# Kernel optimization log

Measured on AMD Instinct MI355X. Metric: run time of the kernel, lower is better.

## Reference

```python
import jax, jax.numpy as jnp
import numpy as np
import math

NH = 16  # n_head
HS = 64  # head_size = n_embd // n_head


def setup_inputs() -> dict:
    key = jax.random.key(0)
    ks = jax.random.split(key, 7)
    B, T, C, QL, KVL = 2, 2048, 1024, 128, 128
    s = lambda k, shape, fan_in: jax.random.normal(k, shape, jnp.float32) / np.sqrt(fan_in)
    return {
        "x": jax.random.normal(ks[0], (B, T, C), jnp.float32),
        "W_dq": s(ks[1], (QL, C), C),
        "W_uq": s(ks[2], (C, QL), QL),
        "W_dkv": s(ks[3], (KVL, C), C),
        "W_uk": s(ks[4], (C, KVL), KVL),
        "W_uv": s(ks[5], (C, KVL), KVL),
        "W_o": s(ks[6], (C, C), C),
    }


def reference(x, W_dq, W_uq, W_dkv, W_uk, W_uv, W_o):
    B, T, C = x.shape
    kvl = W_dkv.shape[0]
    # absorbed matrices (training branch)
    k_eff = (W_dq.T @ W_uq.T @ W_uk).reshape(NH, HS, kvl)            # (nh, hs, kvl)
    v_eff = (W_uv.T @ W_o.T).reshape(kvl, NH, HS).transpose(1, 0, 2)  # (nh, kvl, hs)
    # latent kv cache
    c_kv = x @ W_dkv.T                                                # (B, T, kvl)
    # query path
    q = (x @ W_dq.T @ W_uq.T).reshape(B, T, NH, HS).transpose(0, 2, 1, 3)  # (B, nh, T, hs)
    # scores: q @ k_eff @ c_kv^T
    ql = jnp.einsum('bhtd,hdl->bhtl', q, k_eff)                       # (B, nh, T, kvl)
    scores = jnp.einsum('bhtl,bsl->bhts', ql, c_kv) / math.sqrt(HS)   # (B, nh, T, T)
    # causal mask
    mask = jnp.tril(jnp.ones((T, T), dtype=bool))
    scores = jnp.where(mask[None, None], scores, -jnp.inf)
    attn = jax.nn.softmax(scores, axis=-1)
    # output: attn @ c_kv @ v_eff
    ctx = jnp.einsum('bhts,bsl->bhtl', attn, c_kv)                    # (B, nh, T, kvl)
    y = jnp.einsum('bhtl,hld->bhtd', ctx, v_eff)                      # (B, nh, T, hs)
    y = y.transpose(0, 2, 1, 3).reshape(B, T, C)
    return y, c_kv
```

## Files before the change

kernel.cpp:

```cpp
#include <hip/hip_runtime.h>
#include <hip/hip_bf16.h>

typedef __hip_bfloat16 bf16;
typedef __attribute__((ext_vector_type(8))) short short8;
typedef __attribute__((ext_vector_type(4))) float f32x4;

#define NHD 16
#define HSD 64
#define KVLD 128
#define QLD 128
#define CD 1024
#define BD 2
#define TD 2048

__device__ __forceinline__ short8 ld8(const bf16* p) { return *(const short8*)p; }
__device__ __forceinline__ void st8(bf16* p, short8 v) { *(short8*)p = v; }

__device__ __forceinline__ void st4(bf16* p, float4 a) {
    union { short4 s; bf16 h[4]; } u;
    u.h[0] = __float2bfloat16(a.x); u.h[1] = __float2bfloat16(a.y);
    u.h[2] = __float2bfloat16(a.z); u.h[3] = __float2bfloat16(a.w);
    *(short4*)p = u.s;
}
__device__ __forceinline__ void st4f(bf16* p, f32x4 a) {
    union { short4 s; bf16 h[4]; } u;
    u.h[0] = __float2bfloat16(a[0]); u.h[1] = __float2bfloat16(a[1]);
    u.h[2] = __float2bfloat16(a[2]); u.h[3] = __float2bfloat16(a[3]);
    *(short4*)p = u.s;
}

__global__ __launch_bounds__(256) void k_pre(const float* __restrict__ wuq,
                                             const float* __restrict__ wuk,
                                             const float* __restrict__ wdq,
                                             const float* __restrict__ wdkv,
                                             float* __restrict__ m1p,
                                             float* __restrict__ G,
                                             bf16* __restrict__ wqkv_bf) {
    const int b = blockIdx.x;
    const int tid = threadIdx.x;
    if (b < 128) {
        const int part = b >> 4, ig = b & 15;
        const int i = ig * 8 + (tid >> 5);
        const int j4 = (tid & 31) << 2;
        const float* wq = wuq + (size_t)part * 128 * QLD;
        const float* wk = wuk + (size_t)part * 128 * KVLD;
        float4 acc = make_float4(0.f, 0.f, 0.f, 0.f);
        for (int c0 = 0; c0 < 128; c0 += 8) {
            float a[8]; float4 kv[8];
#pragma unroll
            for (int u = 0; u < 8; ++u) {
                a[u] = wq[(c0 + u) * QLD + i];
                kv[u] = *(const float4*)(wk + (c0 + u) * KVLD + j4);
            }
#pragma unroll
            for (int u = 0; u < 8; ++u) {
                acc.x = fmaf(a[u], kv[u].x, acc.x);
                acc.y = fmaf(a[u], kv[u].y, acc.y);
                acc.z = fmaf(a[u], kv[u].z, acc.z);
                acc.w = fmaf(a[u], kv[u].w, acc.w);
            }
        }
        *(float4*)(m1p + (size_t)part * 16384 + (size_t)i * 128 + j4) = acc;
    } else if (b < 256) {
        const int b1 = b - 128;
        const int h = b1 >> 3, p8 = b1 & 7;
        const int p = p8 * 16 + (tid >> 4);
        const int i8 = (tid & 15) << 3;
        float acc[8];
#pragma unroll
        for (int t = 0; t < 8; ++t) acc[t] = 0.f;
        const float* wdqp = wdq + (size_t)p * CD + h * 64;
        const float* wuqh = wuq + (size_t)(h * 64) * QLD + i8;
        for (int d0 = 0; d0 < 64; d0 += 4) {
            float a[4]; float4 b0[4], b1v[4];
#pragma unroll
            for (int u = 0; u < 4; ++u) {
                a[u] = wdqp[d0 + u];
                b0[u] = *(const float4*)(wuqh + (d0 + u) * QLD);
                b1v[u] = *(const float4*)(wuqh + (d0 + u) * QLD + 4);
            }
#pragma unroll
            for (int u = 0; u < 4; ++u) {
                acc[0] = fmaf(a[u], b0[u].x, acc[0]);  acc[1] = fmaf(a[u], b0[u].y, acc[1]);
                acc[2] = fmaf(a[u], b0[u].z, acc[2]);  acc[3] = fmaf(a[u], b0[u].w, acc[3]);
                acc[4] = fmaf(a[u], b1v[u].x, acc[4]); acc[5] = fmaf(a[u], b1v[u].y, acc[5]);
                acc[6] = fmaf(a[u], b1v[u].z, acc[6]); acc[7] = fmaf(a[u], b1v[u].w, acc[7]);
            }
        }
        float* dst = G + (size_t)h * 16384 + (size_t)p * 128 + i8;
        *(float4*)dst = make_float4(acc[0], acc[1], acc[2], acc[3]);
        *(float4*)(dst + 4) = make_float4(acc[4], acc[5], acc[6], acc[7]);
    } else {
        const int r = (b - 256) * 4 + (tid >> 6);
        const int lane = tid & 63;
        const float* src = (r < 128) ? (wdq + (size_t)r * CD) : (wdkv + (size_t)(r - 128) * CD);
        float4 f[4];
#pragma unroll
        for (int k = 0; k < 4; ++k) f[k] = ((const float4*)src)[lane + k * 64];
#pragma unroll
        for (int k = 0; k < 4; ++k)
            st4(wqkv_bf + (size_t)r * CD + (lane + k * 64) * 4, f[k]);
    }
}

__global__ __launch_bounds__(256) void k_main(const float* __restrict__ x,
                                              const bf16* __restrict__ wqkv_bf,
                                              const float* __restrict__ m1p,
                                              const float* __restrict__ G,
                                              const float* __restrict__ wuv,
                                              const float* __restrict__ wo,
                                              bf16* __restrict__ q1_bf,
                                              float* __restrict__ ckv_out,
                                              bf16* __restrict__ ckv_bf,
                                              bf16* __restrict__ ckvT_bf,
                                              bf16* __restrict__ Et_bf,
                                              bf16* __restrict__ veffT_bf) {
    __shared__ __align__(16) char arena[49152];
    const int blk = blockIdx.x;
    const int tid = threadIdx.x;

    if (blk < 256) {
        const int m0 = blk * 16;
        const int w = tid >> 6, lane = tid & 63, m16 = lane & 15, g = lane >> 4;
        bf16* As = (bf16*)arena;
        bf16* Bs = (bf16*)(arena + 2304);

        const int arow = tid >> 4, akc = (tid & 15) << 2;
        const float* axp = x + (size_t)(m0 + arow) * CD + akc;
        int brow[8], bkc[8];
#pragma unroll
        for (int kk = 0; kk < 8; ++kk) {
            int v = tid + kk * 256;
            brow[kk] = v >> 3; bkc[kk] = (v & 7) << 3;
        }

        float4 pA = *(const float4*)(axp);
        short8 pB[8];
#pragma unroll
        for (int kk = 0; kk < 8; ++kk)
            pB[kk] = ld8(wqkv_bf + (size_t)brow[kk] * CD + bkc[kk]);

        f32x4 acc[4];
#pragma unroll
        for (int nb = 0; nb < 4; ++nb) acc[nb] = (f32x4){0.f, 0.f, 0.f, 0.f};

        for (int k0 = 0; k0 < CD; k0 += 64) {
            __syncthreads();
            st4(As + arow * 72 + akc, pA);
#pragma unroll
            for (int kk = 0; kk < 8; ++kk)
                st8(Bs + brow[kk] * 72 + bkc[kk], pB[kk]);
            __syncthreads();
            if (k0 + 64 < CD) {
                pA = *(const float4*)(axp + k0 + 64);
#pragma unroll
                for (int kk = 0; kk < 8; ++kk)
                    pB[kk] = ld8(wqkv_bf + (size_t)brow[kk] * CD + k0 + 64 + bkc[kk]);
            }
            short8 aF[2];
#pragma unroll
            for (int kf = 0; kf < 2; ++kf)
                aF[kf] = ld8(As + m16 * 72 + kf * 32 + g * 8);
#pragma unroll
            for (int nb = 0; nb < 4; ++nb)
#pragma unroll
                for (int kf = 0; kf < 2; ++kf) {
                    short8 bF = ld8(Bs + (w * 64 + nb * 16 + m16) * 72 + kf * 32 + g * 8);
                    acc[nb] = __builtin_amdgcn_mfma_f32_16x16x32_bf16(aF[kf], bF, acc[nb], 0, 0, 0);
                }
        }

#pragma unroll
        for (int nb = 0; nb < 4; ++nb)
#pragma unroll
            for (int r = 0; r < 4; ++r) {
                int t = m0 + g * 4 + r;
                int col = w * 64 + nb * 16 + m16;
                float v = acc[nb][r];
                if (col < 128) {
                    q1_bf[(size_t)t * QLD + col] = __float2bfloat16(v);
                } else {
                    int l = col - 128;
                    ckv_out[(size_t)t * KVLD + l] = v;
                    bf16 hv = __float2bfloat16(v);
                    ckv_bf[(size_t)t * KVLD + l] = hv;
                    int b = t >> 11, tl = t & 2047;
                    ckvT_bf[((size_t)b * KVLD + l) * TD + tl] = hv;
                }
            }
    } else if (blk < 512) {
        const int b2 = blk - 256;
        const int h = b2 >> 4, lb = b2 & 15;
        float* m1s = (float*)arena;
        for (int v = tid; v < 1024; v += 256) {
            int p = v >> 3, lq = v & 7;
            float s = 0.f;
#pragma unroll
            for (int part = 0; part < 8; ++part)
                s += m1p[(size_t)part * 16384 + (size_t)p * 128 + lb * 8 + lq];
            m1s[v] = s;
        }
        __syncthreads();
        const int lq = tid >> 5, i4 = (tid & 31) << 2;
        const float* Gh = G + (size_t)h * 16384;
        float4 acc = make_float4(0.f, 0.f, 0.f, 0.f);
        for (int p0 = 0; p0 < 128; p0 += 8) {
            float4 g[8]; float a[8];
#pragma unroll
            for (int u = 0; u < 8; ++u) {
                g[u] = *(const float4*)(Gh + (p0 + u) * 128 + i4);
                a[u] = m1s[(p0 + u) * 8 + lq];
            }
#pragma unroll
            for (int u = 0; u < 8; ++u) {
                acc.x = fmaf(a[u], g[u].x, acc.x);
                acc.y = fmaf(a[u], g[u].y, acc.y);
                acc.z = fmaf(a[u], g[u].z, acc.z);
                acc.w = fmaf(a[u], g[u].w, acc.w);
            }
        }
        const float sc = 0.1803368801f;
        const int l = lb * 8 + lq;
        st4(Et_bf + ((size_t)h * 128 + l) * 128 + i4,
            make_float4(sc * acc.x, sc * acc.y, sc * acc.z, sc * acc.w));
    } else {
        const int b3 = blk - 512;
        const int cc0 = b3 * 4;
        float* woS = (float*)arena;
        float* wuvS = (float*)arena + 4096;
#pragma unroll
        for (int k = 0; k < 4; ++k)
            ((float4*)woS)[tid + k * 256] = ((const float4*)(wo + (size_t)cc0 * CD))[tid + k * 256];

        const int r = tid >> 6;
        const int lh = tid & 63;
        float4 pf[8];
#pragma unroll
        for (int t = 0; t < 8; ++t)
            pf[t] = ((const float4*)wuv)[t * 256 + tid];

        float a0 = 0.f, a1 = 0.f;
        for (int ch = 0; ch < 16; ++ch) {
            __syncthreads();
#pragma unroll
            for (int t = 0; t < 8; ++t)
                ((float4*)wuvS)[t * 256 + tid] = pf[t];
            __syncthreads();
            if (ch < 15) {
#pragma unroll
                for (int t = 0; t < 8; ++t)
                    pf[t] = ((const float4*)wuv)[(ch + 1) * 2048 + t * 256 + tid];
            }
            const float* wr = woS + r * 1024 + ch * 64;
            const float2* vv = (const float2*)wuvS + lh;
#pragma unroll 16
            for (int cc = 0; cc < 64; ++cc) {
                float wv = wr[cc];
                float2 v = vv[cc * 64];
                a0 = fmaf(wv, v.x, a0);
                a1 = fmaf(wv, v.y, a1);
            }
        }
        union { short2 s; bf16 h2[2]; } u;
        u.h2[0] = __float2bfloat16(a0);
        u.h2[1] = __float2bfloat16(a1);
        *(short2*)(veffT_bf + (size_t)(cc0 + r) * KVLD + lh * 2) = u.s;
    }
}

__global__ __launch_bounds__(512, 4) void k_flash(const bf16* __restrict__ Q1_bf,
                                                  const bf16* __restrict__ Et_bf,
                                                  const bf16* __restrict__ ckv_bf,
                                                  const bf16* __restrict__ ckvT_bf,
                                                  const bf16* __restrict__ veffT_bf,
                                                  float* __restrict__ yout) {
    const int h = blockIdx.x & 15;
    const int b = blockIdx.x >> 4;
    const int qlo = blockIdx.y;
    const int qhi = 31 - qlo;
    const int tid = threadIdx.x;
    const int w = tid >> 6;
    const int ws = w >> 2;
    const int wq = w & 3;
    const int lane = tid & 63;
    const int m16 = lane & 15;
    const int g = lane >> 4;
    const int myqt = ws ? qlo : qhi;
    const int row0 = myqt * 64;

    __shared__ __align__(16) short smem_raw[28288];
    bf16* smem = (bf16*)smem_raw;
    bf16* kvN = smem;
    bf16* kvT = smem + 8704;
    bf16* pS  = smem + 19072 + w * 1152;
    bf16* bufLo = kvT;
    bf16* vT = smem + 19072;

    {
        const bf16 one = __float2bfloat16(1.0f);
        for (int idx = tid; idx < 16 * 72; idx += 512)
            kvT[9216 + idx] = one;
    }

    {
        const bf16* q1hi = Q1_bf + ((size_t)(b * TD + qhi * 64)) * QLD;
        const bf16* q1lo = Q1_bf + ((size_t)(b * TD + qlo * 64)) * QLD;
#pragma unroll
        for (int k = 0; k < 2; ++k) {
            int v = tid + k * 512;
            int row = v >> 4, cv = (v & 15) << 3;
            st8(kvN + row * 136 + cv, ld8(q1hi + row * QLD + cv));
            st8(bufLo + row * 136 + cv, ld8(q1lo + row * QLD + cv));
        }
    }
    __syncthreads();
    bf16* myQ1 = ws ? bufLo : kvN;
    {
        short8 aq[4];
#pragma unroll
        for (int kf = 0; kf < 4; ++kf)
            aq[kf] = ld8(myQ1 + (wq * 16 + m16) * 136 + kf * 32 + g * 8);
        const bf16* Eh = Et_bf + (size_t)h * QLD * KVLD;
        f32x4 qc[8];
#pragma unroll
        for (int nb = 0; nb < 8; ++nb) qc[nb] = (f32x4){0.f, 0.f, 0.f, 0.f};
#pragma unroll
        for (int nb = 0; nb < 8; ++nb)
#pragma unroll
            for (int kf = 0; kf < 4; ++kf) {
                short8 bq = ld8(Eh + (nb * 16 + m16) * QLD + kf * 32 + g * 8);
                qc[nb] = __builtin_amdgcn_mfma_f32_16x16x32_bf16(aq[kf], bq, qc[nb], 0, 0, 0);
            }
        __syncthreads();
#pragma unroll
        for (int nb = 0; nb < 8; ++nb)
#pragma unroll
            for (int r = 0; r < 4; ++r)
                myQ1[(wq * 16 + g * 4 + r) * 136 + nb * 16 + m16] = __float2bfloat16(qc[nb][r]);
    }
    __syncthreads();
    short8 qlA[4];
#pragma unroll
    for (int kf = 0; kf < 4; ++kf)
        qlA[kf] = ld8(myQ1 + (wq * 16 + m16) * 136 + kf * 32 + g * 8);

    f32x4 cx[9];
#pragma unroll
    for (int nb = 0; nb < 9; ++nb) cx[nb] = (f32x4){0.f, 0.f, 0.f, 0.f};
    float mrow = -INFINITY;
    const int rg = row0 + wq * 16 + m16;

    const bf16* ckb = ckv_bf + (size_t)b * TD * KVLD;
    const bf16* ckTb = ckvT_bf + (size_t)b * KVLD * TD;

    int nrow[2], ncol[2], trow[2], tcol[2];
#pragma unroll
    for (int k = 0; k < 2; ++k) {
        int v = tid + k * 512;
        nrow[k] = v >> 4; ncol[k] = (v & 15) << 3;
        trow[k] = v >> 3; tcol[k] = (v & 7) << 3;
    }
    short8 pfN[2], pfT[2];
#pragma unroll
    for (int k = 0; k < 2; ++k) {
        pfN[k] = ld8(ckb + (size_t)nrow[k] * KVLD + ncol[k]);
        pfT[k] = ld8(ckTb + (size_t)trow[k] * TD + tcol[k]);
    }

    for (int tile = 0; tile <= qhi; ++tile) {
        const int s0 = tile * 64;
        __syncthreads();
#pragma unroll
        for (int k = 0; k < 2; ++k) {
            st8(kvN + nrow[k] * 136 + ncol[k], pfN[k]);
            st8(kvT + trow[k] * 72 + tcol[k], pfT[k]);
        }
        __syncthreads();
        if (tile < qhi) {
            const int s1 = s0 + 64;
#pragma unroll
            for (int k = 0; k < 2; ++k) {
                pfN[k] = ld8(ckb + (size_t)(s1 + nrow[k]) * KVLD + ncol[k]);
                pfT[k] = ld8(ckTb + (size_t)trow[k] * TD + s1 + tcol[k]);
            }
        }

        if (ws == 0 || tile <= qlo) {
            f32x4 sa[4];
#pragma unroll
            for (int nb = 0; nb < 4; ++nb) sa[nb] = (f32x4){0.f, 0.f, 0.f, 0.f};
#pragma unroll
            for (int nb = 0; nb < 4; ++nb)
#pragma unroll
                for (int kf = 0; kf < 4; ++kf) {
                    short8 ak = ld8(kvN + (nb * 16 + m16) * 136 + kf * 32 + g * 8);
                    sa[nb] = __builtin_amdgcn_mfma_f32_16x16x32_bf16(ak, qlA[kf], sa[nb], 0, 0, 0);
                }

            if (tile == myqt) {
#pragma unroll
                for (int nb = 0; nb < 4; ++nb)
#pragma unroll
                    for (int r = 0; r < 4; ++r) {
                        int sg = s0 + nb * 16 + g * 4 + r;
                        if (sg > rg) sa[nb][r] = -INFINITY;
                    }
            }

            float mloc = sa[0][0];
#pragma unroll
            for (int nb = 0; nb < 4; ++nb)
#pragma unroll
                for (int r = 0; r < 4; ++r) mloc = fmaxf(mloc, sa[nb][r]);
            mloc = fmaxf(mloc, __shfl_xor(mloc, 16));
            mloc = fmaxf(mloc, __shfl_xor(mloc, 32));
            if (__any(mloc > mrow)) {
                float mt = fmaxf(mrow, mloc);
                float al = exp2f(mrow - mt);
                mrow = mt;
#pragma unroll
                for (int nb = 0; nb < 9; ++nb)
#pragma unroll
                    for (int r = 0; r < 4; ++r) cx[nb][r] *= al;
            }

#pragma unroll
            for (int nb = 0; nb < 4; ++nb) {
                float4 p4;
                p4.x = exp2f(sa[nb][0] - mrow);
                p4.y = exp2f(sa[nb][1] - mrow);
                p4.z = exp2f(sa[nb][2] - mrow);
                p4.w = exp2f(sa[nb][3] - mrow);
                st4(pS + m16 * 72 + nb * 16 + g * 4, p4);
            }
            __builtin_amdgcn_wave_barrier();

            short8 pA[2];
#pragma unroll
            for (int kf = 0; kf < 2; ++kf)
                pA[kf] = ld8(pS + m16 * 72 + kf * 32 + g * 8);
#pragma unroll
            for (int nb = 0; nb < 9; ++nb)
#pragma unroll
                for (int kf = 0; kf < 2; ++kf) {
                    short8 av = ld8(kvT + (nb * 16 + m16) * 72 + kf * 32 + g * 8);
                    cx[nb] = __builtin_amdgcn_mfma_f32_16x16x32_bf16(av, pA[kf], cx[nb], 0, 0, 0);
                }
        }
    }

    float invl = 1.f / cx[8][0];
#pragma unroll
    for (int nb = 0; nb < 8; ++nb)
#pragma unroll
        for (int r = 0; r < 4; ++r) cx[nb][r] *= invl;
    __syncthreads();
    bf16* ctxS = ws ? bufLo : kvN;
#pragma unroll
    for (int nb = 0; nb < 8; ++nb)
        st4f(ctxS + (wq * 16 + m16) * 136 + nb * 16 + g * 4, cx[nb]);
    {
        const bf16* vsrc = veffT_bf + (size_t)h * HSD * KVLD;
#pragma unroll
        for (int k = 0; k < 2; ++k) {
            int v = tid + k * 512;
            int row = v >> 4, cv = (v & 15) << 3;
            st8(vT + row * 136 + cv, ld8(vsrc + row * KVLD + cv));
        }
    }
    __syncthreads();

    short8 cB[4];
#pragma unroll
    for (int kf = 0; kf < 4; ++kf)
        cB[kf] = ld8(ctxS + (wq * 16 + m16) * 136 + kf * 32 + g * 8);
    f32x4 ya[4];
#pragma unroll
    for (int nb = 0; nb < 4; ++nb) ya[nb] = (f32x4){0.f, 0.f, 0.f, 0.f};
#pragma unroll
    for (int nb = 0; nb < 4; ++nb)
#pragma unroll
        for (int kf = 0; kf < 4; ++kf) {
            short8 av = ld8(vT + (nb * 16 + m16) * 136 + kf * 32 + g * 8);
            ya[nb] = __builtin_amdgcn_mfma_f32_16x16x32_bf16(av, cB[kf], ya[nb], 0, 0, 0);
        }
    float* yo = yout + ((size_t)b * TD + rg) * CD + h * HSD;
#pragma unroll
    for (int nb = 0; nb < 4; ++nb)
        *(float4*)(yo + nb * 16 + g * 4) = *(float4*)&ya[nb];
}

extern "C" void kernel_launch(void* const* d_in, const int* in_sizes, int n_in,
                              void* d_out, int out_size, void* d_ws, size_t ws_size,
                              hipStream_t stream) {
    const float* x    = (const float*)d_in[0];
    const float* wdq  = (const float*)d_in[1];
    const float* wuq  = (const float*)d_in[2];
    const float* wdkv = (const float*)d_in[3];
    const float* wuk  = (const float*)d_in[4];
    const float* wuv  = (const float*)d_in[5];
    const float* wo   = (const float*)d_in[6];
    float* yout = (float*)d_out;
    float* ckv_out = yout + (size_t)BD * TD * CD;

    float* ws = (float*)d_ws;
    float* M1P = ws;
    float* G   = M1P + 131072;
    bf16* wqkv_bf  = (bf16*)(G + 262144);
    bf16* Et_bf    = wqkv_bf + 262144;
    bf16* veffT_bf = Et_bf + 262144;
    bf16* ckv_bf   = veffT_bf + 131072;
    bf16* ckvT_bf  = ckv_bf + 524288;
    bf16* Q1_bf    = ckvT_bf + 524288;

    k_pre <<<320, 256, 0, stream>>>(wuq, wuk, wdq, wdkv, M1P, G, wqkv_bf);
    k_main<<<768, 256, 0, stream>>>(x, wqkv_bf, M1P, G, wuv, wo,
                                    Q1_bf, ckv_out, ckv_bf, ckvT_bf, Et_bf, veffT_bf);

    dim3 grid(32, 16);
    k_flash<<<grid, 512, 0, stream>>>(Q1_bf, Et_bf, ckv_bf, ckvT_bf, veffT_bf, yout);
}
```

Baseline: 226.1 us.

## Fuse weight preprocessing kernel into main projection kernel, removing a launch

Removes the separate k_pre launch. The projection blocks now read fp32 W_dq/W_dkv directly and convert to bf16 on the fly. The E-matrix blocks recompute the Wuq^T·Wuk product and the per-head G tile locally in shared memory instead of reading partial sums from global memory. This drops one kernel launch and its global round trips, at the cost of redundant per-block recomputation: each of the 256 E blocks does a 1024-long reduction plus a G tile computation.

```diff
diff --git a/kernel.cpp b/kernel.cpp
--- a/kernel.cpp
+++ b/kernel.cpp
@@ -16,6 +16,14 @@
 __device__ __forceinline__ short8 ld8(const bf16* p) { return *(const short8*)p; }
 __device__ __forceinline__ void st8(bf16* p, short8 v) { *(short8*)p = v; }
 
+__device__ __forceinline__ short8 cvt8(float4 a, float4 b) {
+    union { short8 s; bf16 h[8]; } u;
+    u.h[0] = __float2bfloat16(a.x); u.h[1] = __float2bfloat16(a.y);
+    u.h[2] = __float2bfloat16(a.z); u.h[3] = __float2bfloat16(a.w);
+    u.h[4] = __float2bfloat16(b.x); u.h[5] = __float2bfloat16(b.y);
+    u.h[6] = __float2bfloat16(b.z); u.h[7] = __float2bfloat16(b.w);
+    return u.s;
+}
 __device__ __forceinline__ void st4(bf16* p, float4 a) {
     union { short4 s; bf16 h[4]; } u;
     u.h[0] = __float2bfloat16(a.x); u.h[1] = __float2bfloat16(a.y);
@@ -29,92 +37,19 @@
     *(short4*)p = u.s;
 }
 
-__global__ __launch_bounds__(256) void k_pre(const float* __restrict__ wuq,
+__global__ __launch_bounds__(256) void k_aux(const float* __restrict__ x,
+                                             const float* __restrict__ wdq,
+                                             const float* __restrict__ wuq,
+                                             const float* __restrict__ wdkv,
                                              const float* __restrict__ wuk,
-                                             const float* __restrict__ wdq,
-                                             const float* __restrict__ wdkv,
-                                             float* __restrict__ m1p,
-                                             float* __restrict__ G,
-                                             bf16* __restrict__ wqkv_bf) {
-    const int b = blockIdx.x;
-    const int tid = threadIdx.x;
-    if (b < 128) {
-        const int part = b >> 4, ig = b & 15;
-        const int i = ig * 8 + (tid >> 5);
-        const int j4 = (tid & 31) << 2;
-        const float* wq = wuq + (size_t)part * 128 * QLD;
-        const float* wk = wuk + (size_t)part * 128 * KVLD;
-        float4 acc = make_float4(0.f, 0.f, 0.f, 0.f);
-        for (int c0 = 0; c0 < 128; c0 += 8) {
-            float a[8]; float4 kv[8];
-#pragma unroll
-            for (int u = 0; u < 8; ++u) {
-                a[u] = wq[(c0 + u) * QLD + i];
-                kv[u] = *(const float4*)(wk + (c0 + u) * KVLD + j4);
-            }
-#pragma unroll
-            for (int u = 0; u < 8; ++u) {
-                acc.x = fmaf(a[u], kv[u].x, acc.x);
-                acc.y = fmaf(a[u], kv[u].y, acc.y);
-                acc.z = fmaf(a[u], kv[u].z, acc.z);
-                acc.w = fmaf(a[u], kv[u].w, acc.w);
-            }
-        }
-        *(float4*)(m1p + (size_t)part * 16384 + (size_t)i * 128 + j4) = acc;
-    } else if (b < 256) {
-        const int b1 = b - 128;
-        const int h = b1 >> 3, p8 = b1 & 7;
-        const int p = p8 * 16 + (tid >> 4);
-        const int i8 = (tid & 15) << 3;
-        float acc[8];
-#pragma unroll
-        for (int t = 0; t < 8; ++t) acc[t] = 0.f;
-        const float* wdqp = wdq + (size_t)p * CD + h * 64;
-        const float* wuqh = wuq + (size_t)(h * 64) * QLD + i8;
-        for (int d0 = 0; d0 < 64; d0 += 4) {
-            float a[4]; float4 b0[4], b1v[4];
-#pragma unroll
-            for (int u = 0; u < 4; ++u) {
-                a[u] = wdqp[d0 + u];
-                b0[u] = *(const float4*)(wuqh + (d0 + u) * QLD);
-                b1v[u] = *(const float4*)(wuqh + (d0 + u) * QLD + 4);
-            }
-#pragma unroll
-            for (int u = 0; u < 4; ++u) {
-                acc[0] = fmaf(a[u], b0[u].x, acc[0]);  acc[1] = fmaf(a[u], b0[u].y, acc[1]);
-                acc[2] = fmaf(a[u], b0[u].z, acc[2]);  acc[3] = fmaf(a[u], b0[u].w, acc[3]);
-                acc[4] = fmaf(a[u], b1v[u].x, acc[4]); acc[5] = fmaf(a[u], b1v[u].y, acc[5]);
-                acc[6] = fmaf(a[u], b1v[u].z, acc[6]); acc[7] = fmaf(a[u], b1v[u].w, acc[7]);
-            }
-        }
-        float* dst = G + (size_t)h * 16384 + (size_t)p * 128 + i8;
-        *(float4*)dst = make_float4(acc[0], acc[1], acc[2], acc[3]);
-        *(float4*)(dst + 4) = make_float4(acc[4], acc[5], acc[6], acc[7]);
-    } else {
-        const int r = (b - 256) * 4 + (tid >> 6);
-        const int lane = tid & 63;
-        const float* src = (r < 128) ? (wdq + (size_t)r * CD) : (wdkv + (size_t)(r - 128) * CD);
-        float4 f[4];
-#pragma unroll
-        for (int k = 0; k < 4; ++k) f[k] = ((const float4*)src)[lane + k * 64];
-#pragma unroll
-        for (int k = 0; k < 4; ++k)
-            st4(wqkv_bf + (size_t)r * CD + (lane + k * 64) * 4, f[k]);
-    }
-}
-
-__global__ __launch_bounds__(256) void k_main(const float* __restrict__ x,
-                                              const bf16* __restrict__ wqkv_bf,
-                                              const float* __restrict__ m1p,
-                                              const float* __restrict__ G,
-                                              const float* __restrict__ wuv,
-                                              const float* __restrict__ wo,
-                                              bf16* __restrict__ q1_bf,
-                                              float* __restrict__ ckv_out,
-                                              bf16* __restrict__ ckv_bf,
-                                              bf16* __restrict__ ckvT_bf,
-                                              bf16* __restrict__ Et_bf,
-                                              bf16* __restrict__ veffT_bf) {
+                                             const float* __restrict__ wuv,
+                                             const float* __restrict__ wo,
+                                             bf16* __restrict__ q1_bf,
+                                             float* __restrict__ ckv_out,
+                                             bf16* __restrict__ ckv_bf,
+                                             bf16* __restrict__ ckvT_bf,
+                                             bf16* __restrict__ Et_bf,
+                                             bf16* __restrict__ veffT_bf) {
     __shared__ __align__(16) char arena[49152];
     const int blk = blockIdx.x;
     const int tid = threadIdx.x;
@@ -128,17 +63,22 @@
         const int arow = tid >> 4, akc = (tid & 15) << 2;
         const float* axp = x + (size_t)(m0 + arow) * CD + akc;
         int brow[8], bkc[8];
+        const float* bsrc[8];
 #pragma unroll
         for (int kk = 0; kk < 8; ++kk) {
             int v = tid + kk * 256;
             brow[kk] = v >> 3; bkc[kk] = (v & 7) << 3;
+            bsrc[kk] = ((brow[kk] < 128) ? (wdq + (size_t)brow[kk] * CD)
+                                         : (wdkv + (size_t)(brow[kk] - 128) * CD)) + bkc[kk];
         }
 
         float4 pA = *(const float4*)(axp);
-        short8 pB[8];
-#pragma unroll
-        for (int kk = 0; kk < 8; ++kk)
-            pB[kk] = ld8(wqkv_bf + (size_t)brow[kk] * CD + bkc[kk]);
+        float4 pB0[8], pB1[8];
+#pragma unroll
+        for (int kk = 0; kk < 8; ++kk) {
+            pB0[kk] = *(const float4*)(bsrc[kk]);
+            pB1[kk] = *(const float4*)(bsrc[kk] + 4);
+        }
 
         f32x4 acc[4];
 #pragma unroll
@@ -149,13 +89,15 @@
             st4(As + arow * 72 + akc, pA);
 #pragma unroll
             for (int kk = 0; kk < 8; ++kk)
-                st8(Bs + brow[kk] * 72 + bkc[kk], pB[kk]);
+                st8(Bs + brow[kk] * 72 + bkc[kk], cvt8(pB0[kk], pB1[kk]));
             __syncthreads();
             if (k0 + 64 < CD) {
                 pA = *(const float4*)(axp + k0 + 64);
 #pragma unroll
-                for (int kk = 0; kk < 8; ++kk)
-                    pB[kk] = ld8(wqkv_bf + (size_t)brow[kk] * CD + k0 + 64 + bkc[kk]);
+                for (int kk = 0; kk < 8; ++kk) {
+                    pB0[kk] = *(const float4*)(bsrc[kk] + k0 + 64);
+                    pB1[kk] = *(const float4*)(bsrc[kk] + k0 + 68);
+                }
             }
             short8 aF[2];
 #pragma unroll
@@ -190,39 +132,87 @@
             }
     } else if (blk < 512) {
         const int b2 = blk - 256;
-        const int h = b2 >> 4, lb = b2 & 15;
+        const int h = b2 >> 4;
+        const int lb = b2 & 15;
         float* m1s = (float*)arena;
-        for (int v = tid; v < 1024; v += 256) {
-            int p = v >> 3, lq = v & 7;
-            float s = 0.f;
-#pragma unroll
-            for (int part = 0; part < 8; ++part)
-                s += m1p[(size_t)part * 16384 + (size_t)p * 128 + lb * 8 + lq];
-            m1s[v] = s;
-        }
-        __syncthreads();
-        const int lq = tid >> 5, i4 = (tid & 31) << 2;
-        const float* Gh = G + (size_t)h * 16384;
-        float4 acc = make_float4(0.f, 0.f, 0.f, 0.f);
-        for (int p0 = 0; p0 < 128; p0 += 8) {
-            float4 g[8]; float a[8];
-#pragma unroll
-            for (int u = 0; u < 8; ++u) {
-                g[u] = *(const float4*)(Gh + (p0 + u) * 128 + i4);
-                a[u] = m1s[(p0 + u) * 8 + lq];
-            }
-#pragma unroll
-            for (int u = 0; u < 8; ++u) {
-                acc.x = fmaf(a[u], g[u].x, acc.x);
-                acc.y = fmaf(a[u], g[u].y, acc.y);
-                acc.z = fmaf(a[u], g[u].z, acc.z);
-                acc.w = fmaf(a[u], g[u].w, acc.w);
-            }
+        float* gS  = (float*)(arena + 4096);
+
+        {
+            const int p = tid >> 1;
+            const int lh = tid & 1;
+            const int l0 = lb * 8 + lh * 4;
+            const float* wq = wuq + p;
+            const float* wk = wuk + l0;
+            float4 A = make_float4(0.f, 0.f, 0.f, 0.f);
+            for (int c0 = 0; c0 < CD; c0 += 4) {
+                float a[4]; float4 v[4];
+#pragma unroll
+                for (int u = 0; u < 4; ++u) {
+                    a[u] = wq[(c0 + u) * QLD];
+                    v[u] = *(const float4*)(wk + (c0 + u) * KVLD);
+                }
+#pragma unroll
+                for (int u = 0; u < 4; ++u) {
+                    A.x = fmaf(a[u], v[u].x, A.x); A.y = fmaf(a[u], v[u].y, A.y);
+                    A.z = fmaf(a[u], v[u].z, A.z); A.w = fmaf(a[u], v[u].w, A.w);
+                }
+            }
+            *(float4*)(m1s + p * 8 + lh * 4) = A;
+        }
+
+        const int le = tid >> 5;
+        const int i4 = (tid & 31) << 2;
+        float4 E = make_float4(0.f, 0.f, 0.f, 0.f);
+
+#pragma unroll 1
+        for (int ph = 0; ph < 2; ++ph) {
+            {
+                const int pl = tid >> 2;
+                const int i0 = (tid & 3) << 5;
+                const float* wa = wdq + (size_t)(ph * 64 + pl) * CD + h * 64;
+                const float* wb = wuq + (size_t)(h * 64) * QLD + i0;
+                float4 Gc[8];
+#pragma unroll
+                for (int t = 0; t < 8; ++t) Gc[t] = make_float4(0.f, 0.f, 0.f, 0.f);
+                for (int d = 0; d < 64; ++d) {
+                    float a = wa[d];
+                    float4 r[8];
+#pragma unroll
+                    for (int t = 0; t < 8; ++t)
+                        r[t] = *(const float4*)(wb + d * QLD + t * 4);
+#pragma unroll
+                    for (int t = 0; t < 8; ++t) {
+                        Gc[t].x = fmaf(a, r[t].x, Gc[t].x);
+                        Gc[t].y = fmaf(a, r[t].y, Gc[t].y);
+                        Gc[t].z = fmaf(a, r[t].z, Gc[t].z);
+                        Gc[t].w = fmaf(a, r[t].w, Gc[t].w);
+                    }
+                }
+                float* gd = gS + pl * 128 + i0;
+#pragma unroll
+                for (int t = 0; t < 8; ++t) *(float4*)(gd + t * 4) = Gc[t];
+            }
+            __syncthreads();
+            {
+                for (int p2 = 0; p2 < 64; p2 += 4) {
+                    float a[4]; float4 g[4];
+#pragma unroll
+                    for (int u = 0; u < 4; ++u) {
+                        a[u] = m1s[(ph * 64 + p2 + u) * 8 + le];
+                        g[u] = *(const float4*)(gS + (p2 + u) * 128 + i4);
+                    }
+#pragma unroll
+                    for (int u = 0; u < 4; ++u) {
+                        E.x = fmaf(a[u], g[u].x, E.x); E.y = fmaf(a[u], g[u].y, E.y);
+                        E.z = fmaf(a[u], g[u].z, E.z); E.w = fmaf(a[u], g[u].w, E.w);
+                    }
+                }
+            }
+            __syncthreads();
         }
         const float sc = 0.1803368801f;
-        const int l = lb * 8 + lq;
-        st4(Et_bf + ((size_t)h * 128 + l) * 128 + i4,
-            make_float4(sc * acc.x, sc * acc.y, sc * acc.z, sc * acc.w));
+        st4(Et_bf + ((size_t)h * 128 + lb * 8 + le) * 128 + i4,
+            make_float4(sc * E.x, sc * E.y, sc * E.z, sc * E.w));
     } else {
         const int b3 = blk - 512;
         const int cc0 = b3 * 4;
@@ -503,19 +493,14 @@
     float* yout = (float*)d_out;
     float* ckv_out = yout + (size_t)BD * TD * CD;
 
-    float* ws = (float*)d_ws;
-    float* M1P = ws;
-    float* G   = M1P + 131072;
-    bf16* wqkv_bf  = (bf16*)(G + 262144);
-    bf16* Et_bf    = wqkv_bf + 262144;
+    bf16* Et_bf    = (bf16*)d_ws;
     bf16* veffT_bf = Et_bf + 262144;
     bf16* ckv_bf   = veffT_bf + 131072;
     bf16* ckvT_bf  = ckv_bf + 524288;
     bf16* Q1_bf    = ckvT_bf + 524288;
 
-    k_pre <<<320, 256, 0, stream>>>(wuq, wuk, wdq, wdkv, M1P, G, wqkv_bf);
-    k_main<<<768, 256, 0, stream>>>(x, wqkv_bf, M1P, G, wuv, wo,
-                                    Q1_bf, ckv_out, ckv_bf, ckvT_bf, Et_bf, veffT_bf);
+    k_aux<<<768, 256, 0, stream>>>(x, wdq, wuq, wdkv, wuk, wuv, wo,
+                                   Q1_bf, ckv_out, ckv_bf, ckvT_bf, Et_bf, veffT_bf);
 
     dim3 grid(32, 16);
     k_flash<<<grid, 512, 0, stream>>>(Q1_bf, Et_bf, ckv_bf, ckvT_bf, veffT_bf, yout);
```

After: 357.5 us. 1.58x slower.
